# Kernel tuning notes

Measured on AMD Instinct MI355X. Metric: run time of the kernel, lower is better.

## Reference

```python
import jax, jax.numpy as jnp
import numpy as np
from jax import lax

WS = (4, 8, 8)        # window_size (D,H,W)
DIM = 128
HEADS = 4
HD = DIM // HEADS      # 32
SCALE = HD ** -0.5     # swinv1, lif neuron -> head_dim**-0.5
TAU = 2.0
VTH = 1.0
ALPHA = 2.0            # ATan surrogate width


def _rel_pos_index(ws):
    # static numpy computation of relative_position_index, shape (N, N)
    coords = np.stack(np.meshgrid(np.arange(ws[0]), np.arange(ws[1]), np.arange(ws[2]), indexing='ij'))
    cf = coords.reshape(3, -1)                      # (3, N)
    rel = (cf[:, :, None] - cf[:, None, :]).transpose(1, 2, 0).astype(np.int64)  # (N,N,3)
    rel[:, :, 0] += ws[0] - 1
    rel[:, :, 1] += ws[1] - 1
    rel[:, :, 2] += ws[2] - 1
    rel[:, :, 0] *= (2 * ws[1] - 1) * (2 * ws[2] - 1)
    rel[:, :, 1] *= 2 * ws[2] - 1
    return rel.sum(-1)

RPI = _rel_pos_index(WS)  # (N, N) int


@jax.custom_vjp
def spike(x):
    return (x >= 0.0).astype(x.dtype)

def _spike_fwd(x):
    return spike(x), x

def _spike_bwd(x, g):
    # ATan surrogate gradient (spikingjelly default)
    return (g * (ALPHA / (2.0 * (1.0 + (np.pi / 2.0 * ALPHA * x) ** 2))),)

spike.defvjp(_spike_fwd, _spike_bwd)


def lif(x):
    # multi-step LIF over leading time axis: v' = v + (x - v)/tau, hard reset to 0
    def step(v, xt):
        v = v + (xt - v) / TAU
        s = spike(v - VTH)
        return v * (1.0 - s), s
    return lax.scan(step, jnp.zeros_like(x[0]), x)[1]


def setup_inputs() -> dict:
    key = jax.random.key(0)
    ks = jax.random.split(key, 7)
    x = jax.random.normal(ks[0], (WS[0], 256, WS[1], WS[2], DIM), dtype=jnp.float32)
    Wq = jax.random.normal(ks[1], (DIM, DIM), dtype=jnp.float32) * 0.02
    Wk = jax.random.normal(ks[2], (DIM, DIM), dtype=jnp.float32) * 0.02
    Wv = jax.random.normal(ks[3], (DIM, DIM), dtype=jnp.float32) * 0.02
    rpb_table = jax.random.normal(ks[4], ((2 * WS[0] - 1) * (2 * WS[1] - 1) * (2 * WS[2] - 1), HEADS), dtype=jnp.float32) * 0.02
    Wproj = jax.random.normal(ks[5], (DIM, DIM), dtype=jnp.float32) * 0.02
    bproj = jax.random.normal(ks[6], (DIM,), dtype=jnp.float32) * 0.02
    return {"x": x, "Wq": Wq, "Wk": Wk, "Wv": Wv, "rpb_table": rpb_table, "Wproj": Wproj, "bproj": bproj}


def reference(x, Wq, Wk, Wv, rpb_table, Wproj, bproj):
    T, B_, H, W, C = x.shape
    N = T * H * W
    # QKV: linear (no bias) -> spiking neuron over time axis
    q = lif(jnp.einsum('tbhwc,dc->tbhwd', x, Wq))
    k = lif(jnp.einsum('tbhwc,dc->tbhwd', x, Wk))
    v = lif(jnp.einsum('tbhwc,dc->tbhwd', x, Wv))
    # literal row-major reshape as in torch: (T,B_,H,W,C) -> (B_, heads, N, hd)
    q = q.reshape(B_, HEADS, N, HD)
    k = k.reshape(B_, HEADS, N, HD)
    v = v.reshape(B_, HEADS, N, HD)
    # scaled QK^T (NO softmax in the original forward)
    attn = jnp.einsum('bhnd,bhmd->bhnm', q * SCALE, k)
    rpb = rpb_table[RPI.reshape(-1)].reshape(N, N, HEADS).transpose(2, 0, 1)  # (heads,N,N)
    attn = attn + rpb[None]
    out = jnp.einsum('bhnm,bhmd->bhnd', attn, v)
    out = out.reshape(B_, HEADS, T, H, W, HD).transpose(2, 0, 3, 4, 1, 5).reshape(T, B_, H, W, C)
    out = jnp.einsum('tbhwc,dc->tbhwd', out, Wproj) + bproj
    out = lif(out).reshape(B_, N, C)
    return (out, attn)
```

## Files before the change

kernel.cpp:

```cpp
#include <hip/hip_runtime.h>
#include <hip/hip_bf16.h>


typedef __attribute__((ext_vector_type(8))) short bf16x8;
typedef __attribute__((ext_vector_type(4))) float f32x4;

#define MFMA16(a, b, c) __builtin_amdgcn_mfma_f32_16x16x32_bf16((a), (b), (c), 0, 0, 0)

__device__ __forceinline__ unsigned short f2bf(float f) {
    union { __hip_bfloat16 h; unsigned short u; } cv;
    cv.h = __float2bfloat16(f);
    return cv.u;
}

__device__ __forceinline__ void cvt8_store(unsigned short* dst, const float* src) {
    float4 f0 = *(const float4*)(src);
    float4 f1 = *(const float4*)(src + 4);
    unsigned short h[8];
    h[0] = f2bf(f0.x); h[1] = f2bf(f0.y); h[2] = f2bf(f0.z); h[3] = f2bf(f0.w);
    h[4] = f2bf(f1.x); h[5] = f2bf(f1.y); h[6] = f2bf(f1.z); h[7] = f2bf(f1.w);
    *(uint4*)dst = *(const uint4*)h;
}

__global__ __launch_bounds__(256) void k_qkv_lif(
    const float* __restrict__ x,
    const float* __restrict__ Wq,
    const float* __restrict__ Wk,
    const float* __restrict__ Wv,
    const float* __restrict__ tbl,
    unsigned int* __restrict__ qbits,
    unsigned int* __restrict__ kbits,
    unsigned int* __restrict__ vbits,
    float* __restrict__ rpbx)
{
    if (blockIdx.y == 3) {
        int base = blockIdx.x * 1024 + threadIdx.x * 4;
        int hh = base >> 16;
        int n = (base >> 8) & 255, m0 = base & 255;
        int zn = n >> 6, yn = (n >> 3) & 7, xn = n & 7;
        float4 o;
#pragma unroll
        for (int i = 0; i < 4; ++i) {
            int m = m0 + i;
            int zm = m >> 6, ym = (m >> 3) & 7, xm = m & 7;
            int ri = (zn - zm + 3) * 225 + (yn - ym + 7) * 15 + (xn - xm + 7);
            ((float*)&o)[i] = tbl[ri * 4 + hh];
        }
        *(float4*)&rpbx[base] = o;
        return;
    }

    __shared__ unsigned short Wl[128 * 136];
    __shared__ unsigned short Xl[64 * 136];

    const int tid = threadIdx.x;
    const int wv = tid >> 6, lane = tid & 63;
    const int l15 = lane & 15, lh = lane >> 4;
    const int wsel = blockIdx.y;
    const float* W = (wsel == 0) ? Wq : (wsel == 1) ? Wk : Wv;
    unsigned int* bits = (wsel == 0) ? qbits : (wsel == 1) ? kbits : vbits;
    const int B = blockIdx.x;

    {
#pragma unroll
        for (int i = 0; i < 8; ++i) {
            int e = i * 2048 + tid * 8;
            int r = e >> 7, cc = e & 127;
            cvt8_store(&Wl[r * 136 + cc], W + r * 128 + cc);
        }
    }

    f32x4 vst[8];
#pragma unroll
    for (int nt = 0; nt < 8; ++nt) vst[nt] = (f32x4){0.f, 0.f, 0.f, 0.f};

    for (int t = 0; t < 4; ++t) {
        __syncthreads();
        const float* xg = x + t * 2097152 + B * 8192;
#pragma unroll
        for (int i = 0; i < 4; ++i) {
            int e = i * 2048 + tid * 8;
            int r = e >> 7, cc = e & 127;
            cvt8_store(&Xl[r * 136 + cc], xg + r * 128 + cc);
        }
        __syncthreads();

        f32x4 acc[8];
#pragma unroll
        for (int nt = 0; nt < 8; ++nt) acc[nt] = (f32x4){0.f, 0.f, 0.f, 0.f};
#pragma unroll
        for (int kk = 0; kk < 4; ++kk) {
            bf16x8 a = *(const bf16x8*)&Xl[(wv * 16 + l15) * 136 + kk * 32 + lh * 8];
#pragma unroll
            for (int nt = 0; nt < 8; ++nt) {
                bf16x8 b = *(const bf16x8*)&Wl[(nt * 16 + l15) * 136 + kk * 32 + lh * 8];
                acc[nt] = MFMA16(a, b, acc[nt]);
            }
        }
        unsigned short sp[8][4];
#pragma unroll
        for (int nt = 0; nt < 8; ++nt) {
#pragma unroll
            for (int reg = 0; reg < 4; ++reg) {
                float y = acc[nt][reg];
                float v = vst[nt][reg];
                v = v + (y - v) * 0.5f;
                float s = (v >= 1.0f) ? 1.0f : 0.0f;
                vst[nt][reg] = v * (1.0f - s);
                sp[nt][reg] = (s != 0.0f) ? (unsigned short)1 : (unsigned short)0;
            }
        }
        __syncthreads();
#pragma unroll
        for (int nt = 0; nt < 8; ++nt)
#pragma unroll
            for (int reg = 0; reg < 4; ++reg)
                Xl[(wv * 16 + lh * 4 + reg) * 136 + nt * 16 + l15] = sp[nt][reg];
        __syncthreads();
        {
            const unsigned short* rowp = &Xl[(tid >> 2) * 136 + (tid & 3) * 32];
            unsigned int mask = 0;
#pragma unroll
            for (int j8 = 0; j8 < 4; ++j8) {
                uint4 u = *(const uint4*)(rowp + j8 * 8);
                int base = j8 * 8;
                if (u.x & 0xFFFFu) mask |= 1u << (base + 0);
                if (u.x >> 16)     mask |= 1u << (base + 1);
                if (u.y & 0xFFFFu) mask |= 1u << (base + 2);
                if (u.y >> 16)     mask |= 1u << (base + 3);
                if (u.z & 0xFFFFu) mask |= 1u << (base + 4);
                if (u.z >> 16)     mask |= 1u << (base + 5);
                if (u.w & 0xFFFFu) mask |= 1u << (base + 6);
                if (u.w >> 16)     mask |= 1u << (base + 7);
            }
            bits[(t * 256 + B) * 256 + tid] = mask;
        }
    }
}

__global__ __launch_bounds__(256) void k_attn(
    const unsigned int* __restrict__ qbits,
    const unsigned int* __restrict__ kbits,
    const unsigned int* __restrict__ vbits,
    const float* __restrict__ rpbx,
    float* __restrict__ attn_out,
    unsigned short* __restrict__ o_ws)
{
    __shared__ unsigned int  qb[256];
    __shared__ unsigned short vT[32 * 264];
    __shared__ unsigned short attnL[32 * 264];

    const int tid = threadIdx.x;
    const int wv = tid >> 6, lane = tid & 63;
    const int l15 = lane & 15, lh = lane >> 4;
    const int g = blockIdx.x, hh = g & 3;

    qb[tid] = qbits[g * 256 + tid];
    uint4 km = *(const uint4*)&kbits[g * 256 + (tid & 63) * 4];
    {
        unsigned int vb = vbits[g * 256 + tid];
#pragma unroll
        for (int d = 0; d < 32; ++d)
            vT[d * 264 + tid] = ((vb >> d) & 1u) ? (unsigned short)0x3F80
                                                 : (unsigned short)0;
    }
    __syncthreads();

    const float SC = 0.17677669529663687f;
    float* attn_b = attn_out + (size_t)g * 65536;
    const float* rp = rpbx + hh * 65536;
    unsigned short* ob = o_ws + g * 8192;
    const int rg = wv, m0 = (tid & 63) * 4;
    const int rt = wv >> 1, nh = wv & 1;

    for (int c = 0; c < 8; ++c) {
#pragma unroll
        for (int j = 0; j < 8; ++j) {
            int n = c * 32 + j * 4 + rg;
            unsigned int qn = qb[n];
            float4 rp4 = *(const float4*)&rp[n * 256 + m0];
            f32x4 av;
            av.x = (float)__popc(qn & km.x) * SC + rp4.x;
            av.y = (float)__popc(qn & km.y) * SC + rp4.y;
            av.z = (float)__popc(qn & km.z) * SC + rp4.z;
            av.w = (float)__popc(qn & km.w) * SC + rp4.w;
            __builtin_nontemporal_store(av, (f32x4*)(attn_b + n * 256 + m0));
            unsigned int p0 = (unsigned int)f2bf(av.x) | ((unsigned int)f2bf(av.y) << 16);
            unsigned int p1 = (unsigned int)f2bf(av.z) | ((unsigned int)f2bf(av.w) << 16);
            uint2 pk; pk.x = p0; pk.y = p1;
            *(uint2*)&attnL[(j * 4 + rg) * 264 + m0] = pk;
        }
        __syncthreads();
        f32x4 oc = (f32x4){0.f, 0.f, 0.f, 0.f};
#pragma unroll
        for (int kk = 0; kk < 8; ++kk) {
            bf16x8 a = *(const bf16x8*)&attnL[(rt * 16 + l15) * 264 + kk * 32 + lh * 8];
            bf16x8 b = *(const bf16x8*)&vT[(nh * 16 + l15) * 264 + kk * 32 + lh * 8];
            oc = MFMA16(a, b, oc);
        }
#pragma unroll
        for (int reg = 0; reg < 4; ++reg) {
            int n = c * 32 + rt * 16 + lh * 4 + reg;
            ob[n * 32 + nh * 16 + l15] = f2bf(oc[reg]);
        }
        __syncthreads();
    }
}

__global__ __launch_bounds__(256) void k_proj_lif(
    const unsigned short* __restrict__ o_ws,
    const float* __restrict__ Wp,
    const float* __restrict__ bp,
    float* __restrict__ out0)
{
    __shared__ unsigned short Wl[128 * 136];
    __shared__ unsigned short Al[64 * 136];

    const int tid = threadIdx.x;
    const int wv = tid >> 6, lane = tid & 63;
    const int l15 = lane & 15, lh = lane >> 4;
    const int b = blockIdx.x;

    {
#pragma unroll
        for (int i = 0; i < 8; ++i) {
            int e = i * 2048 + tid * 8;
            int r = e >> 7, cc = e & 127;
            cvt8_store(&Wl[r * 136 + cc], Wp + r * 128 + cc);
        }
    }

    float biasf[2];
#pragma unroll
    for (int ntl = 0; ntl < 2; ++ntl)
        biasf[ntl] = bp[(wv * 2 + ntl) * 16 + l15];

    const unsigned short* ob = o_ws + b * 32768;

    for (int c = 0; c < 4; ++c) {
        __syncthreads();
#pragma unroll
        for (int i = 0; i < 4; ++i) {
            int e = i * 2048 + tid * 8;
            int lr2 = e >> 7, cc = e & 127;
            int t2 = lr2 >> 4, rit = lr2 & 15;
            int hhh = cc >> 5, hd = cc & 31;
            int n = t2 * 64 + c * 16 + rit;
            *(uint4*)&Al[lr2 * 136 + cc] =
                *(const uint4*)(ob + (hhh * 256 + n) * 32 + hd);
        }
        __syncthreads();

        f32x4 acc[4][2];
#pragma unroll
        for (int t2 = 0; t2 < 4; ++t2)
#pragma unroll
            for (int ntl = 0; ntl < 2; ++ntl)
                acc[t2][ntl] = (f32x4){0.f, 0.f, 0.f, 0.f};
#pragma unroll
        for (int kk = 0; kk < 4; ++kk) {
            bf16x8 a[4];
#pragma unroll
            for (int t2 = 0; t2 < 4; ++t2)
                a[t2] = *(const bf16x8*)&Al[(t2 * 16 + l15) * 136 + kk * 32 + lh * 8];
#pragma unroll
            for (int ntl = 0; ntl < 2; ++ntl) {
                bf16x8 bb = *(const bf16x8*)&Wl[((wv * 2 + ntl) * 16 + l15) * 136 + kk * 32 + lh * 8];
#pragma unroll
                for (int t2 = 0; t2 < 4; ++t2)
                    acc[t2][ntl] = MFMA16(a[t2], bb, acc[t2][ntl]);
            }
        }
#pragma unroll
        for (int ntl = 0; ntl < 2; ++ntl) {
            int d = (wv * 2 + ntl) * 16 + l15;
#pragma unroll
            for (int reg = 0; reg < 4; ++reg) {
                int hw = c * 16 + lh * 4 + reg;
                float v = 0.f;
#pragma unroll
                for (int t2 = 0; t2 < 4; ++t2) {
                    float y = acc[t2][ntl][reg] + biasf[ntl];
                    v = v + (y - v) * 0.5f;
                    float s = (v >= 1.0f) ? 1.0f : 0.0f;
                    v = v * (1.0f - s);
                    __builtin_nontemporal_store(
                        s, out0 + t2 * 2097152 + b * 8192 + hw * 128 + d);
                }
            }
        }
    }
}

extern "C" void kernel_launch(void* const* d_in, const int* in_sizes, int n_in,
                              void* d_out, int out_size, void* d_ws, size_t ws_size,
                              hipStream_t stream)
{
    const float* x   = (const float*)d_in[0];
    const float* Wq  = (const float*)d_in[1];
    const float* Wk  = (const float*)d_in[2];
    const float* Wv  = (const float*)d_in[3];
    const float* tbl = (const float*)d_in[4];
    const float* Wp  = (const float*)d_in[5];
    const float* bp  = (const float*)d_in[6];

    float* out0 = (float*)d_out;
    float* attn = out0 + 8388608;

    unsigned short* o_ws = (unsigned short*)d_ws;
    unsigned int* qbits = (unsigned int*)(o_ws + 8388608);
    unsigned int* kbits = qbits + 262144;
    unsigned int* vbits = kbits + 262144;
    float* rpbx = (float*)(vbits + 262144);

    k_qkv_lif<<<dim3(256, 4), 256, 0, stream>>>(x, Wq, Wk, Wv, tbl,
                                                qbits, kbits, vbits, rpbx);
    k_attn<<<1024, 256, 0, stream>>>(qbits, kbits, vbits, rpbx, attn, o_ws);
    k_proj_lif<<<256, 256, 0, stream>>>(o_ws, Wp, bp, out0);
}
```

Baseline: 352.7 us.

## Fuse attention and projection kernels via per-batch arrival counter

Merges the attention and projection+LIF kernels into one launch. Each of the four head blocks for a window bumps an atomic counter, and the last one to arrive runs the projection for that window. Shared memory is aliased between the two phases, and the counters are zeroed inside the QKV kernel. This removes one kernel launch and the gap between kernels, but the projection now runs on only a quarter of the blocks, and the block that does it carries a bigger shared-memory footprint, which may lower occupancy.

```diff
diff --git a/kernel.cpp b/kernel.cpp
--- a/kernel.cpp
+++ b/kernel.cpp
@@ -31,9 +31,11 @@
     unsigned int* __restrict__ qbits,
     unsigned int* __restrict__ kbits,
     unsigned int* __restrict__ vbits,
-    float* __restrict__ rpbx)
+    float* __restrict__ rpbx,
+    unsigned int* __restrict__ cnt)
 {
     if (blockIdx.y == 3) {
+        if (blockIdx.x == 0) cnt[threadIdx.x] = 0;
         int base = blockIdx.x * 1024 + threadIdx.x * 4;
         int hh = base >> 16;
         int n = (base >> 8) & 255, m0 = base & 255;
@@ -138,17 +140,25 @@
     }
 }
 
-__global__ __launch_bounds__(256) void k_attn(
+__global__ __launch_bounds__(256) void k_attn_proj(
     const unsigned int* __restrict__ qbits,
     const unsigned int* __restrict__ kbits,
     const unsigned int* __restrict__ vbits,
     const float* __restrict__ rpbx,
+    const float* __restrict__ Wp,
+    const float* __restrict__ bp,
     float* __restrict__ attn_out,
-    unsigned short* __restrict__ o_ws)
+    unsigned short* __restrict__ o_ws,
+    unsigned int* __restrict__ cnt,
+    float* __restrict__ out0)
 {
-    __shared__ unsigned int  qb[256];
-    __shared__ unsigned short vT[32 * 264];
-    __shared__ unsigned short attnL[32 * 264];
+    __shared__ __align__(16) unsigned char smem[52224];
+    __shared__ int winner;
+    unsigned int*   qb    = (unsigned int*)smem;
+    unsigned short* vT    = (unsigned short*)(smem + 1024);
+    unsigned short* attnL = (unsigned short*)(smem + 17920);
+    unsigned short* Wl = (unsigned short*)smem;
+    unsigned short* Al = (unsigned short*)(smem + 34816);
 
     const int tid = threadIdx.x;
     const int wv = tid >> 6, lane = tid & 63;
@@ -205,21 +215,17 @@
         }
         __syncthreads();
     }
-}
-
-__global__ __launch_bounds__(256) void k_proj_lif(
-    const unsigned short* __restrict__ o_ws,
-    const float* __restrict__ Wp,
-    const float* __restrict__ bp,
-    float* __restrict__ out0)
-{
-    __shared__ unsigned short Wl[128 * 136];
-    __shared__ unsigned short Al[64 * 136];
-
-    const int tid = threadIdx.x;
-    const int wv = tid >> 6, lane = tid & 63;
-    const int l15 = lane & 15, lh = lane >> 4;
-    const int b = blockIdx.x;
+
+    const int b = g >> 2;
+    __threadfence();
+    __syncthreads();
+    if (tid == 0) {
+        unsigned int old = atomicAdd(&cnt[b], 1u);
+        winner = (old == 3u) ? 1 : 0;
+    }
+    __syncthreads();
+    if (!winner) return;
+    __threadfence();
 
     {
 #pragma unroll
@@ -229,13 +235,12 @@
             cvt8_store(&Wl[r * 136 + cc], Wp + r * 128 + cc);
         }
     }
-
     float biasf[2];
 #pragma unroll
     for (int ntl = 0; ntl < 2; ++ntl)
         biasf[ntl] = bp[(wv * 2 + ntl) * 16 + l15];
 
-    const unsigned short* ob = o_ws + b * 32768;
+    const unsigned short* obp = o_ws + b * 32768;
 
     for (int c = 0; c < 4; ++c) {
         __syncthreads();
@@ -247,7 +252,7 @@
             int hhh = cc >> 5, hd = cc & 31;
             int n = t2 * 64 + c * 16 + rit;
             *(uint4*)&Al[lr2 * 136 + cc] =
-                *(const uint4*)(ob + (hhh * 256 + n) * 32 + hd);
+                *(const uint4*)(obp + (hhh * 256 + n) * 32 + hd);
         }
         __syncthreads();
 
@@ -312,9 +317,10 @@
     unsigned int* kbits = qbits + 262144;
     unsigned int* vbits = kbits + 262144;
     float* rpbx = (float*)(vbits + 262144);
+    unsigned int* cnt = (unsigned int*)(rpbx + 262144);
 
     k_qkv_lif<<<dim3(256, 4), 256, 0, stream>>>(x, Wq, Wk, Wv, tbl,
-                                                qbits, kbits, vbits, rpbx);
-    k_attn<<<1024, 256, 0, stream>>>(qbits, kbits, vbits, rpbx, attn, o_ws);
-    k_proj_lif<<<256, 256, 0, stream>>>(o_ws, Wp, bp, out0);
-}
+                                                qbits, kbits, vbits, rpbx, cnt);
+    k_attn_proj<<<1024, 256, 0, stream>>>(qbits, kbits, vbits, rpbx, Wp, bp,
+                                          attn, o_ws, cnt, out0);
+}
```

Measured after the change: 609.5 us. 1.73x slower.

## Recompute attention fragments in registers for MFMA, removing shared staging and barriers

Applied to the files above, without the earlier changes.

The attention kernel now writes the fp32 attention matrix in one streaming loop. For the attn@V MFMA it rebuilds the bf16 A-fragments directly in registers from the q/k bitmasks and the relative-position bias, rather than staging them through shared memory. This drops the attnL buffer and the per-chunk __syncthreads pairs, and each wave owns 64 rows with two MFMA accumulators. The cost is recomputing popcounts and re-reading the bias (likely cache hits) and more per-lane scalar LDS reads of kb.

```diff
diff --git a/kernel.cpp b/kernel.cpp
--- a/kernel.cpp
+++ b/kernel.cpp
@@ -147,8 +147,8 @@
     unsigned short* __restrict__ o_ws)
 {
     __shared__ unsigned int  qb[256];
+    __shared__ unsigned int  kb[256];
     __shared__ unsigned short vT[32 * 264];
-    __shared__ unsigned short attnL[32 * 264];
 
     const int tid = threadIdx.x;
     const int wv = tid >> 6, lane = tid & 63;
@@ -156,6 +156,7 @@
     const int g = blockIdx.x, hh = g & 3;
 
     qb[tid] = qbits[g * 256 + tid];
+    kb[tid] = kbits[g * 256 + tid];
     uint4 km = *(const uint4*)&kbits[g * 256 + (tid & 63) * 4];
     {
         unsigned int vb = vbits[g * 256 + tid];
@@ -170,40 +171,54 @@
     float* attn_b = attn_out + (size_t)g * 65536;
     const float* rp = rpbx + hh * 65536;
     unsigned short* ob = o_ws + g * 8192;
-    const int rg = wv, m0 = (tid & 63) * 4;
-    const int rt = wv >> 1, nh = wv & 1;
-
-    for (int c = 0; c < 8; ++c) {
-#pragma unroll
-        for (int j = 0; j < 8; ++j) {
-            int n = c * 32 + j * 4 + rg;
-            unsigned int qn = qb[n];
-            float4 rp4 = *(const float4*)&rp[n * 256 + m0];
-            f32x4 av;
-            av.x = (float)__popc(qn & km.x) * SC + rp4.x;
-            av.y = (float)__popc(qn & km.y) * SC + rp4.y;
-            av.z = (float)__popc(qn & km.z) * SC + rp4.z;
-            av.w = (float)__popc(qn & km.w) * SC + rp4.w;
-            __builtin_nontemporal_store(av, (f32x4*)(attn_b + n * 256 + m0));
-            unsigned int p0 = (unsigned int)f2bf(av.x) | ((unsigned int)f2bf(av.y) << 16);
-            unsigned int p1 = (unsigned int)f2bf(av.z) | ((unsigned int)f2bf(av.w) << 16);
-            uint2 pk; pk.x = p0; pk.y = p1;
-            *(uint2*)&attnL[(j * 4 + rg) * 264 + m0] = pk;
-        }
-        __syncthreads();
-        f32x4 oc = (f32x4){0.f, 0.f, 0.f, 0.f};
+    const int m0 = (tid & 63) * 4;
+
+#pragma unroll 4
+    for (int i = 0; i < 64; ++i) {
+        int n = i * 4 + wv;
+        unsigned int qn = qb[n];
+        float4 rp4 = *(const float4*)&rp[n * 256 + m0];
+        f32x4 av;
+        av.x = (float)__popc(qn & km.x) * SC + rp4.x;
+        av.y = (float)__popc(qn & km.y) * SC + rp4.y;
+        av.z = (float)__popc(qn & km.z) * SC + rp4.z;
+        av.w = (float)__popc(qn & km.w) * SC + rp4.w;
+        __builtin_nontemporal_store(av, (f32x4*)(attn_b + n * 256 + m0));
+    }
+
+#pragma unroll
+    for (int tt = 0; tt < 4; ++tt) {
+        const int nrow = wv * 64 + tt * 16 + l15;
+        const unsigned int qn = qb[nrow];
+        const float* rprow = rp + nrow * 256;
+        f32x4 oc0 = (f32x4){0.f, 0.f, 0.f, 0.f};
+        f32x4 oc1 = (f32x4){0.f, 0.f, 0.f, 0.f};
 #pragma unroll
         for (int kk = 0; kk < 8; ++kk) {
-            bf16x8 a = *(const bf16x8*)&attnL[(rt * 16 + l15) * 264 + kk * 32 + lh * 8];
-            bf16x8 b = *(const bf16x8*)&vT[(nh * 16 + l15) * 264 + kk * 32 + lh * 8];
-            oc = MFMA16(a, b, oc);
+            const int k0 = kk * 32 + lh * 8;
+            unsigned short af[8];
+            float4 r0 = *(const float4*)&rprow[k0];
+            float4 r1 = *(const float4*)&rprow[k0 + 4];
+            af[0] = f2bf((float)__popc(qn & kb[k0 + 0]) * SC + r0.x);
+            af[1] = f2bf((float)__popc(qn & kb[k0 + 1]) * SC + r0.y);
+            af[2] = f2bf((float)__popc(qn & kb[k0 + 2]) * SC + r0.z);
+            af[3] = f2bf((float)__popc(qn & kb[k0 + 3]) * SC + r0.w);
+            af[4] = f2bf((float)__popc(qn & kb[k0 + 4]) * SC + r1.x);
+            af[5] = f2bf((float)__popc(qn & kb[k0 + 5]) * SC + r1.y);
+            af[6] = f2bf((float)__popc(qn & kb[k0 + 6]) * SC + r1.z);
+            af[7] = f2bf((float)__popc(qn & kb[k0 + 7]) * SC + r1.w);
+            bf16x8 a = *(const bf16x8*)af;
+            bf16x8 b0 = *(const bf16x8*)&vT[l15 * 264 + k0];
+            bf16x8 b1 = *(const bf16x8*)&vT[(16 + l15) * 264 + k0];
+            oc0 = MFMA16(a, b0, oc0);
+            oc1 = MFMA16(a, b1, oc1);
         }
 #pragma unroll
         for (int reg = 0; reg < 4; ++reg) {
-            int n = c * 32 + rt * 16 + lh * 4 + reg;
-            ob[n * 32 + nh * 16 + l15] = f2bf(oc[reg]);
-        }
-        __syncthreads();
+            int n = wv * 64 + tt * 16 + lh * 4 + reg;
+            ob[n * 32 + l15]      = f2bf(oc0[reg]);
+            ob[n * 32 + 16 + l15] = f2bf(oc1[reg]);
+        }
     }
 }
 
```

Measured after the change: 372.6 us. 1.06x slower.
